# Kernel tuning notes

Hardware: AMD Instinct MI355X
Metric: run time of the kernel (lower is better)

The kernel has to match this reference:

```python
import jax, jax.numpy as jnp
import numpy as np
import math

N_HEADS = 16
KV_HEADS = 4
HEAD_DIM = 128
ROPE_BASE = 1000000.0


def _make_rope(seq_len, dim, base=ROPE_BASE):
    inv_freq = 1.0 / (base ** (np.arange(0, dim, 2, dtype=np.float32) / dim))
    t = np.arange(seq_len, dtype=np.float32)
    freqs = np.outer(t, inv_freq)                     # [S, dim/2]
    emb = np.concatenate([freqs, freqs], axis=-1)     # [S, dim]
    return jnp.asarray(np.cos(emb)), jnp.asarray(np.sin(emb))


def setup_inputs() -> dict:
    key = jax.random.key(0)
    ks = jax.random.split(key, 6)
    B, S, H = 2, 2048, 2048
    kv_dim = KV_HEADS * HEAD_DIM
    s = 1.0 / math.sqrt(H)
    x = jax.random.normal(ks[0], (B, S, H), jnp.float32)
    wq = jax.random.normal(ks[1], (H, H), jnp.float32) * s
    wk = jax.random.normal(ks[2], (kv_dim, H), jnp.float32) * s
    wv = jax.random.normal(ks[3], (kv_dim, H), jnp.float32) * s
    wo = jax.random.normal(ks[4], (H, H), jnp.float32) * s
    bq = jnp.zeros((H,), jnp.float32)
    bk = jnp.zeros((kv_dim,), jnp.float32)
    bv = jnp.zeros((kv_dim,), jnp.float32)
    bo = jnp.zeros((H,), jnp.float32)
    cos, sin = _make_rope(S, HEAD_DIM)
    return {"x": x, "wq": wq, "bq": bq, "wk": wk, "bk": bk,
            "wv": wv, "bv": bv, "wo": wo, "bo": bo, "cos": cos, "sin": sin}


def _rotate_half(t):
    half = t.shape[-1] // 2
    return jnp.concatenate([-t[..., half:], t[..., :half]], axis=-1)


def reference(x, wq, bq, wk, bk, wv, bv, wo, bo, cos, sin):
    B, S, H = x.shape
    hd, nh, kvh = HEAD_DIM, N_HEADS, KV_HEADS
    rep = nh // kvh

    q = (x @ wq.T + bq).reshape(B, S, nh, hd)
    k = (x @ wk.T + bk).reshape(B, S, kvh, hd)
    v = (x @ wv.T + bv).reshape(B, S, kvh, hd)

    # RoPE (rotate-half), cos/sin: [S, hd] -> broadcast over batch and heads
    c = cos[None, :, None, :]
    s_ = sin[None, :, None, :]
    q = q * c + _rotate_half(q) * s_
    k = k * c + _rotate_half(k) * s_

    # GQA: expand KV heads by rep
    k = jnp.repeat(k, rep, axis=2)   # [B, S, nh, hd]
    v = jnp.repeat(v, rep, axis=2)

    q = q.transpose(0, 2, 1, 3)      # [B, nh, S, hd]
    k = k.transpose(0, 2, 1, 3)
    v = v.transpose(0, 2, 1, 3)

    score = jnp.einsum('bhqd,bhkd->bhqk', q, k) / math.sqrt(hd)
    causal = jnp.triu(jnp.full((S, S), -jnp.inf, jnp.float32), k=1)
    score = score + causal
    attn = jax.nn.softmax(score.astype(jnp.float32), axis=-1).astype(q.dtype)

    out = jnp.einsum('bhqk,bhkd->bhqd', attn, v)   # [B, nh, S, hd]
    out = out.transpose(0, 2, 1, 3).reshape(B, S, nh * hd)
    return out @ wo.T + bo
```

## Files before the change

### kernel.cpp

```cpp
#include <hip/hip_runtime.h>

typedef unsigned short u16;
typedef __bf16 bf16x8 __attribute__((ext_vector_type(8)));
typedef float  f32x4  __attribute__((ext_vector_type(4)));

#define SEQ 2048

__device__ __forceinline__ float bf2f(u16 u) {
    union { unsigned int i; float f; } c;
    c.i = ((unsigned int)u) << 16;
    return c.f;
}
__device__ __forceinline__ u16 f2bf(float f) {
    union { float f; unsigned int i; } c;
    c.f = f;
    unsigned int u = c.i;
    u += 0x7FFFu + ((u >> 16) & 1u);
    return (u16)(u >> 16);
}

__device__ __forceinline__ void gl_lds16(const u16* g, u16* l) {
    __builtin_amdgcn_global_load_lds(
        (const __attribute__((address_space(1))) unsigned int*)(g),
        (__attribute__((address_space(3))) unsigned int*)(l), 16, 0, 0);
}

__device__ __forceinline__ void cvt4(const float* s, u16* d) {
    float4 v = *(const float4*)s;
    ushort4 o;
    o.x = f2bf(v.x); o.y = f2bf(v.y); o.z = f2bf(v.z); o.w = f2bf(v.w);
    *(ushort4*)d = o;
}

__global__ void prep(const float* __restrict__ x,
                     const float* __restrict__ wq, const float* __restrict__ wk,
                     const float* __restrict__ wv,
                     const float* __restrict__ bq, const float* __restrict__ bk,
                     const float* __restrict__ bv,
                     u16* __restrict__ xb, u16* __restrict__ wqkvb,
                     float* __restrict__ biasb)
{
    const int E0 = 2097152;
    const int E1 = E0 + 1048576;
    const int E2 = E1 + 262144;
    const int E3 = E2 + 262144;
    const int E4 = E3 + 768;
    int i = blockIdx.x * blockDim.x + threadIdx.x;
    int stride = gridDim.x * blockDim.x;
    for (; i < E4; i += stride) {
        if (i < E0)      cvt4(x  + (size_t)i * 4,        xb    + (size_t)i * 4);
        else if (i < E1) cvt4(wq + (size_t)(i - E0) * 4, wqkvb + (size_t)(i - E0) * 4);
        else if (i < E2) cvt4(wk + (size_t)(i - E1) * 4, wqkvb + 4194304 + (size_t)(i - E1) * 4);
        else if (i < E3) cvt4(wv + (size_t)(i - E2) * 4, wqkvb + 5242880 + (size_t)(i - E2) * 4);
        else {
            int j = i - E3;
            const float* src = (j < 512) ? (bq + j * 4)
                             : (j < 640) ? (bk + (j - 512) * 4)
                                         : (bv + (j - 640) * 4);
            *(float4*)&biasb[j * 4] = *(const float4*)src;
        }
    }
}

__global__ void cvt_f32_bf16(const float* __restrict__ in, u16* __restrict__ out, int n4) {
    int i = blockIdx.x * blockDim.x + threadIdx.x;
    int stride = gridDim.x * blockDim.x;
    for (; i < n4; i += stride) cvt4(in + (size_t)i * 4, out + (size_t)i * 4);
}

template<int MODE>
__global__ __launch_bounds__(256) void gemm_bt(
    const u16* __restrict__ A, const u16* __restrict__ B,
    const float* __restrict__ bias, float* __restrict__ C,
    u16* __restrict__ qb, u16* __restrict__ kb, u16* __restrict__ vt,
    int M, int N, int K)
{
    __shared__ __align__(16) u16 lA[128 * 32];
    __shared__ __align__(16) u16 lB[128 * 32];
    const int tid   = threadIdx.x;
    const int lane  = tid & 63;
    const int wave  = tid >> 6;
    const int waveM = (wave >> 1) * 64;
    const int waveN = (wave & 1) * 64;
    const int bm = blockIdx.x * 128;
    const int bn = blockIdx.y * 128;
    const int lrow = lane & 15;
    const int koff = (lane >> 4) * 8;

    f32x4 acc[4][4] = {};

    for (int k0 = 0; k0 < K; k0 += 32) {
        __syncthreads();
#pragma unroll
        for (int p = 0; p < 2; ++p) {
            int idx = p * 256 + tid;
            int row = idx >> 2;
            int ch  = idx & 3;
            gl_lds16(&A[(size_t)(bm + row) * K + k0 + ch * 8], &lA[(p * 256 + wave * 64) * 8]);
            gl_lds16(&B[(size_t)(bn + row) * K + k0 + ch * 8], &lB[(p * 256 + wave * 64) * 8]);
        }
        __syncthreads();

        bf16x8 af[4], bfr[4];
#pragma unroll
        for (int i = 0; i < 4; ++i)
            af[i] = *(const bf16x8*)&lA[(waveM + i * 16 + lrow) * 32 + koff];
#pragma unroll
        for (int j = 0; j < 4; ++j)
            bfr[j] = *(const bf16x8*)&lB[(waveN + j * 16 + lrow) * 32 + koff];
#pragma unroll
        for (int i = 0; i < 4; ++i)
#pragma unroll
            for (int j = 0; j < 4; ++j)
                acc[i][j] = __builtin_amdgcn_mfma_f32_16x16x32_bf16(
                    af[i], bfr[j], acc[i][j], 0, 0, 0);
    }

    const int r4 = (lane >> 4) * 4;
    const int cn = lane & 15;
#pragma unroll
    for (int i = 0; i < 4; ++i) {
#pragma unroll
        for (int j = 0; j < 4; ++j) {
            int row0 = bm + waveM + i * 16 + r4;
            int col  = bn + waveN + j * 16 + cn;
            float bc = bias[col];
#pragma unroll
            for (int r = 0; r < 4; ++r) {
                float val = acc[i][j][r] + bc;
                if (MODE == 0) {
                    C[(size_t)(row0 + r) * N + col] = val;
                } else {
                    int row = row0 + r;
                    int b = row >> 11;
                    int s = row & 2047;
                    int d = col & 127;
                    u16 o = f2bf(val);
                    if (col < 2048) {
                        int h = col >> 7;
                        qb[(((size_t)(b * 16 + h) * SEQ) + s) * 128 + d] = o;
                    } else if (col < 2560) {
                        int h = (col - 2048) >> 7;
                        kb[(((size_t)(b * 4 + h) * SEQ) + s) * 128 + d] = o;
                    } else {
                        int h = (col - 2560) >> 7;
                        vt[(((size_t)(b * 4 + h) * 128) + d) * SEQ + s] = o;
                    }
                }
            }
        }
    }
}

__global__ void rope_inplace(u16* __restrict__ qb, u16* __restrict__ kb,
                             const float* __restrict__ cosb, const float* __restrict__ sinb)
{
    const int n = (65536 + 16384) * 64;
    int i = blockIdx.x * blockDim.x + threadIdx.x;
    if (i >= n) return;
    int d0  = i & 63;
    int row = i >> 6;
    u16* base;
    if (row < 65536) base = qb + (size_t)row * 128;
    else             base = kb + (size_t)(row - 65536) * 128;
    int s = row & (SEQ - 1);
    float c  = cosb[s * 128 + d0];
    float sn = sinb[s * 128 + d0];
    float a0 = bf2f(base[d0]);
    float a1 = bf2f(base[d0 + 64]);
    base[d0]      = f2bf(a0 * c - a1 * sn);
    base[d0 + 64] = f2bf(a1 * c + a0 * sn);
}

__global__ __launch_bounds__(256, 2) void attn_mfma(
    const u16* __restrict__ qb, const u16* __restrict__ kb,
    const u16* __restrict__ vt, u16* __restrict__ ob)
{
    __shared__ __align__(16) u16 Ks[2][4][64][32];
    __shared__ __align__(16) u16 Vts[2][2][128][32];
    __shared__ __align__(16) u16 Ph[4][16][64];

    const int pair = blockIdx.x;
    const int qA   = pair, qB = 31 - pair;
    const int h    = blockIdx.y;
    const int b    = blockIdx.z;
    const int kvh  = h >> 2;
    const int tid  = threadIdx.x;
    const int lane = tid & 63;
    const int w    = tid >> 6;
    const int c16  = lane & 15;
    const int quad = lane >> 4;
    const float qscale = 0.08838834764831845f * 1.4426950408889634f;

    const u16* kbase  = kb + ((size_t)(b * 4 + kvh) * SEQ) * 128;
    const u16* vtbase = vt + ((size_t)(b * 4 + kvh) * 128) * SEQ;

    bf16x8 qfA[4], qfB[4];
    {
        const u16* qpA = qb + (((size_t)(b * 16 + h)) * SEQ + qA * 64 + w * 16 + c16) * 128;
        const u16* qpB = qb + (((size_t)(b * 16 + h)) * SEQ + qB * 64 + w * 16 + c16) * 128;
#pragma unroll
        for (int kk = 0; kk < 4; ++kk) {
            bf16x8 ta = *(const bf16x8*)(qpA + kk * 32 + quad * 8);
            bf16x8 tb = *(const bf16x8*)(qpB + kk * 32 + quad * 8);
#pragma unroll
            for (int e = 0; e < 8; ++e) {
                ta[e] = (__bf16)((float)ta[e] * qscale);
                tb[e] = (__bf16)((float)tb[e] * qscale);
            }
            qfA[kk] = ta; qfB[kk] = tb;
        }
    }

    int ksrc[4], vsrc[4];
#pragma unroll
    for (int it = 0; it < 4; ++it) {
        int o  = (it * 4 + w) * 1024 + lane * 16;
        int kk = o >> 12;
        int r  = (o >> 6) & 63;
        int c  = (o >> 4) & 3;
        ksrc[it] = r * 128 + kk * 32 + c * 8;
        int p2 = o >> 13;
        int d  = (o >> 6) & 127;
        vsrc[it] = d * SEQ + p2 * 32 + c * 8;
    }

    const int nB = qB + 1;
    const int rowLA = qA * 64 + w * 16 + quad * 4;
    const int rowLB = qB * 64 + w * 16 + quad * 4;

    f32x4 oA[8] = {}, oB[8] = {};
    float lA[4] = {}, lB[4] = {};

    u16* KsF  = &Ks[0][0][0][0];
    u16* VtsF = &Vts[0][0][0][0];

    asm volatile("s_waitcnt vmcnt(0)" ::: "memory");

#pragma unroll
    for (int it = 0; it < 4; ++it) {
        gl_lds16(kbase  + ksrc[it], KsF  + (it * 4 + w) * 512);
        gl_lds16(vtbase + vsrc[it], VtsF + (it * 4 + w) * 512);
    }

    for (int kt = 0; kt < nB; ++kt) {
        const int cur = kt & 1;
        if (kt + 1 < nB) {
            const u16* kg = kbase  + (size_t)(kt + 1) * (64 * 128);
            const u16* vg = vtbase + (kt + 1) * 64;
            u16* kd = KsF  + ((kt + 1) & 1) * (4 * 64 * 32);
            u16* vd = VtsF + ((kt + 1) & 1) * (2 * 128 * 32);
#pragma unroll
            for (int it = 0; it < 4; ++it) {
                gl_lds16(kg + ksrc[it], kd + (it * 4 + w) * 512);
                gl_lds16(vg + vsrc[it], vd + (it * 4 + w) * 512);
            }
            asm volatile("s_waitcnt vmcnt(8)" ::: "memory");
        } else {
            asm volatile("s_waitcnt vmcnt(0)" ::: "memory");
        }
        __builtin_amdgcn_s_barrier();
        asm volatile("" ::: "memory");

        const u16* Kb = KsF  + cur * (4 * 64 * 32);
        const u16* Vb = VtsF + cur * (2 * 128 * 32);
        const bool doA = kt <= qA;

        f32x4 sA[4] = {}, sB[4] = {};
        __builtin_amdgcn_s_setprio(1);
        if (doA) {
#pragma unroll
            for (int kk = 0; kk < 4; ++kk)
#pragma unroll
                for (int j = 0; j < 4; ++j) {
                    bf16x8 kf = *(const bf16x8*)(Kb + (size_t)(kk * 64 + j * 16 + c16) * 32 + quad * 8);
                    sA[j] = __builtin_amdgcn_mfma_f32_16x16x32_bf16(qfA[kk], kf, sA[j], 0, 0, 0);
                    sB[j] = __builtin_amdgcn_mfma_f32_16x16x32_bf16(qfB[kk], kf, sB[j], 0, 0, 0);
                }
        } else {
#pragma unroll
            for (int kk = 0; kk < 4; ++kk)
#pragma unroll
                for (int j = 0; j < 4; ++j) {
                    bf16x8 kf = *(const bf16x8*)(Kb + (size_t)(kk * 64 + j * 16 + c16) * 32 + quad * 8);
                    sB[j] = __builtin_amdgcn_mfma_f32_16x16x32_bf16(qfB[kk], kf, sB[j], 0, 0, 0);
                }
        }
        __builtin_amdgcn_s_setprio(0);

        if (doA && kt == qA) {
#pragma unroll
            for (int j = 0; j < 4; ++j)
#pragma unroll
                for (int rr = 0; rr < 4; ++rr)
                    if (kt * 64 + j * 16 + c16 > rowLA + rr) sA[j][rr] = -1e30f;
        }
        if (kt == qB) {
#pragma unroll
            for (int j = 0; j < 4; ++j)
#pragma unroll
                for (int rr = 0; rr < 4; ++rr)
                    if (kt * 64 + j * 16 + c16 > rowLB + rr) sB[j][rr] = -1e30f;
        }

        bf16x8 paA[2], paB[2];
        if (doA) {
#pragma unroll
            for (int jj = 0; jj < 4; ++jj)
#pragma unroll
                for (int rr = 0; rr < 4; ++rr) {
                    float p = __builtin_amdgcn_exp2f(sA[jj][rr]);
                    lA[rr] += p;
                    int row = quad * 4 + rr;
                    Ph[w][row][(((jj * 2 + (c16 >> 3)) + row) & 7) * 8 + (c16 & 7)] = f2bf(p);
                }
#pragma unroll
            for (int k2 = 0; k2 < 2; ++k2)
                paA[k2] = *(const bf16x8*)&Ph[w][c16][(((k2 * 4 + quad) + c16) & 7) * 8];
        }
#pragma unroll
        for (int jj = 0; jj < 4; ++jj)
#pragma unroll
            for (int rr = 0; rr < 4; ++rr) {
                float p = __builtin_amdgcn_exp2f(sB[jj][rr]);
                lB[rr] += p;
                int row = quad * 4 + rr;
                Ph[w][row][(((jj * 2 + (c16 >> 3)) + row) & 7) * 8 + (c16 & 7)] = f2bf(p);
            }
#pragma unroll
        for (int k2 = 0; k2 < 2; ++k2)
            paB[k2] = *(const bf16x8*)&Ph[w][c16][(((k2 * 4 + quad) + c16) & 7) * 8];

        __builtin_amdgcn_s_setprio(1);
        if (doA) {
#pragma unroll
            for (int k2 = 0; k2 < 2; ++k2)
#pragma unroll
                for (int nt = 0; nt < 8; ++nt) {
                    bf16x8 vf = *(const bf16x8*)(Vb + (size_t)(k2 * 128 + nt * 16 + c16) * 32 + quad * 8);
                    oA[nt] = __builtin_amdgcn_mfma_f32_16x16x32_bf16(paA[k2], vf, oA[nt], 0, 0, 0);
                    oB[nt] = __builtin_amdgcn_mfma_f32_16x16x32_bf16(paB[k2], vf, oB[nt], 0, 0, 0);
                }
        } else {
#pragma unroll
            for (int k2 = 0; k2 < 2; ++k2)
#pragma unroll
                for (int nt = 0; nt < 8; ++nt) {
                    bf16x8 vf = *(const bf16x8*)(Vb + (size_t)(k2 * 128 + nt * 16 + c16) * 32 + quad * 8);
                    oB[nt] = __builtin_amdgcn_mfma_f32_16x16x32_bf16(paB[k2], vf, oB[nt], 0, 0, 0);
                }
        }
        __builtin_amdgcn_s_setprio(0);

        asm volatile("" ::: "memory");
        __builtin_amdgcn_s_barrier();
    }

    float liA[4], liB[4];
#pragma unroll
    for (int rr = 0; rr < 4; ++rr) {
        float la = lA[rr], lb = lB[rr];
        la += __shfl_xor(la, 1); lb += __shfl_xor(lb, 1);
        la += __shfl_xor(la, 2); lb += __shfl_xor(lb, 2);
        la += __shfl_xor(la, 4); lb += __shfl_xor(lb, 4);
        la += __shfl_xor(la, 8); lb += __shfl_xor(lb, 8);
        liA[rr] = 1.0f / la;     liB[rr] = 1.0f / lb;
    }
    const size_t rowGA = (size_t)b * SEQ + rowLA;
    const size_t rowGB = (size_t)b * SEQ + rowLB;
#pragma unroll
    for (int nt = 0; nt < 8; ++nt)
#pragma unroll
        for (int rr = 0; rr < 4; ++rr) {
            ob[(rowGA + rr) * 2048 + h * 128 + nt * 16 + c16] = f2bf(oA[nt][rr] * liA[rr]);
            ob[(rowGB + rr) * 2048 + h * 128 + nt * 16 + c16] = f2bf(oB[nt][rr] * liB[rr]);
        }
}

extern "C" void kernel_launch(void* const* d_in, const int* in_sizes, int n_in,
                              void* d_out, int out_size, void* d_ws, size_t ws_size,
                              hipStream_t stream) {
    const float* x    = (const float*)d_in[0];
    const float* wq   = (const float*)d_in[1];
    const float* bq   = (const float*)d_in[2];
    const float* wk   = (const float*)d_in[3];
    const float* bk   = (const float*)d_in[4];
    const float* wv   = (const float*)d_in[5];
    const float* bv   = (const float*)d_in[6];
    const float* wo   = (const float*)d_in[7];
    const float* bo   = (const float*)d_in[8];
    const float* cosb = (const float*)d_in[9];
    const float* sinb = (const float*)d_in[10];
    float* out = (float*)d_out;

    char* ws = (char*)d_ws;
    const size_t OFF_WQKV = 0;
    const size_t OFF_BIAS = 12582912;
    const size_t OFF_QB   = 12599296;
    const size_t OFF_KB   = 29376512;
    const size_t OFF_VT   = 33570816;
    const size_t OFF_XB   = 37765120;

    u16*   wqkvb = (u16*)(ws + OFF_WQKV);
    u16*   wob   = (u16*)(ws + OFF_WQKV);
    float* biasb = (float*)(ws + OFF_BIAS);
    u16*   qb2   = (u16*)(ws + OFF_QB);
    u16*   kb2   = (u16*)(ws + OFF_KB);
    u16*   vt2   = (u16*)(ws + OFF_VT);
    u16*   xb    = (u16*)(ws + OFF_XB);
    u16*   attnb = (u16*)(ws + OFF_XB);

    prep<<<4096, 256, 0, stream>>>(x, wq, wk, wv, bq, bk, bv, xb, wqkvb, biasb);

    gemm_bt<1><<<dim3(32, 24), 256, 0, stream>>>(xb, wqkvb, biasb, nullptr,
                                                 qb2, kb2, vt2, 4096, 3072, 2048);

    cvt_f32_bf16<<<4096, 256, 0, stream>>>(wo, wob, 1048576);

    rope_inplace<<<((65536 + 16384) * 64) / 256, 256, 0, stream>>>(qb2, kb2, cosb, sinb);

    attn_mfma<<<dim3(16, 16, 2), 256, 0, stream>>>(qb2, kb2, vt2, attnb);

    gemm_bt<0><<<dim3(32, 16), 256, 0, stream>>>(attnb, wob, bo, out,
                                                 nullptr, nullptr, nullptr, 4096, 2048, 2048);
}
```

Measured before the change: 377.9 us.

## Remap attention grid per XCD for K/V L2 reuse and simplify sync

Flattens the attention grid to 1D and decodes the block id so its low three bits select (batch, kv-head). With round-robin dispatch across the 8 XCDs, each XCD then serves the query heads and tiles that share the same K/V, which is meant to raise L2 hit rates. The hand-placed s_waitcnt/s_barrier pipeline and s_setprio hints are replaced by plain __syncthreads, which still lets the next tile's prefetch overlap the current compute. The manual float-to-bf16 rounding for P is replaced by the native __bf16 conversion to cut ALU work. The trade-off is less precise control over wait counts, since a full wait now happens at the end of every iteration.

```diff
diff --git a/kernel.cpp b/kernel.cpp
--- a/kernel.cpp
+++ b/kernel.cpp
@@ -180,11 +180,16 @@
     __shared__ __align__(16) u16 Vts[2][2][128][32];
     __shared__ __align__(16) u16 Ph[4][16][64];
 
-    const int pair = blockIdx.x;
+    const int id   = blockIdx.x;
+    const int s8   = id & 7;
+    const int n    = id >> 3;
+    const int pair = n & 15;
+    const int h_lo = n >> 4;
+    const int b    = s8 >> 2;
+    const int kvh  = s8 & 3;
+    const int h    = kvh * 4 + h_lo;
     const int qA   = pair, qB = 31 - pair;
-    const int h    = blockIdx.y;
-    const int b    = blockIdx.z;
-    const int kvh  = h >> 2;
+
     const int tid  = threadIdx.x;
     const int lane = tid & 63;
     const int w    = tid >> 6;
@@ -235,16 +240,16 @@
     u16* KsF  = &Ks[0][0][0][0];
     u16* VtsF = &Vts[0][0][0][0];
 
-    asm volatile("s_waitcnt vmcnt(0)" ::: "memory");
-
 #pragma unroll
     for (int it = 0; it < 4; ++it) {
         gl_lds16(kbase  + ksrc[it], KsF  + (it * 4 + w) * 512);
         gl_lds16(vtbase + vsrc[it], VtsF + (it * 4 + w) * 512);
     }
+    __syncthreads();
 
     for (int kt = 0; kt < nB; ++kt) {
         const int cur = kt & 1;
+
         if (kt + 1 < nB) {
             const u16* kg = kbase  + (size_t)(kt + 1) * (64 * 128);
             const u16* vg = vtbase + (kt + 1) * 64;
@@ -255,25 +260,17 @@
                 gl_lds16(kg + ksrc[it], kd + (it * 4 + w) * 512);
                 gl_lds16(vg + vsrc[it], vd + (it * 4 + w) * 512);
             }
-            asm volatile("s_waitcnt vmcnt(8)" ::: "memory");
-        } else {
-            asm volatile("s_waitcnt vmcnt(0)" ::: "memory");
-        }
-        __builtin_amdgcn_s_barrier();
-        asm volatile("" ::: "memory");
-
-        const u16* Kb = KsF  + cur * (4 * 64 * 32);
-        const u16* Vb = VtsF + cur * (2 * 128 * 32);
+        }
+
         const bool doA = kt <= qA;
 
         f32x4 sA[4] = {}, sB[4] = {};
-        __builtin_amdgcn_s_setprio(1);
         if (doA) {
 #pragma unroll
             for (int kk = 0; kk < 4; ++kk)
 #pragma unroll
                 for (int j = 0; j < 4; ++j) {
-                    bf16x8 kf = *(const bf16x8*)(Kb + (size_t)(kk * 64 + j * 16 + c16) * 32 + quad * 8);
+                    bf16x8 kf = *(const bf16x8*)&Ks[cur][kk][j * 16 + c16][quad * 8];
                     sA[j] = __builtin_amdgcn_mfma_f32_16x16x32_bf16(qfA[kk], kf, sA[j], 0, 0, 0);
                     sB[j] = __builtin_amdgcn_mfma_f32_16x16x32_bf16(qfB[kk], kf, sB[j], 0, 0, 0);
                 }
@@ -282,11 +279,10 @@
             for (int kk = 0; kk < 4; ++kk)
 #pragma unroll
                 for (int j = 0; j < 4; ++j) {
-                    bf16x8 kf = *(const bf16x8*)(Kb + (size_t)(kk * 64 + j * 16 + c16) * 32 + quad * 8);
+                    bf16x8 kf = *(const bf16x8*)&Ks[cur][kk][j * 16 + c16][quad * 8];
                     sB[j] = __builtin_amdgcn_mfma_f32_16x16x32_bf16(qfB[kk], kf, sB[j], 0, 0, 0);
                 }
         }
-        __builtin_amdgcn_s_setprio(0);
 
         if (doA && kt == qA) {
 #pragma unroll
@@ -312,7 +308,7 @@
                     float p = __builtin_amdgcn_exp2f(sA[jj][rr]);
                     lA[rr] += p;
                     int row = quad * 4 + rr;
-                    Ph[w][row][(((jj * 2 + (c16 >> 3)) + row) & 7) * 8 + (c16 & 7)] = f2bf(p);
+                    *(__bf16*)&Ph[w][row][(((jj * 2 + (c16 >> 3)) + row) & 7) * 8 + (c16 & 7)] = (__bf16)p;
                 }
 #pragma unroll
             for (int k2 = 0; k2 < 2; ++k2)
@@ -325,19 +321,18 @@
                 float p = __builtin_amdgcn_exp2f(sB[jj][rr]);
                 lB[rr] += p;
                 int row = quad * 4 + rr;
-                Ph[w][row][(((jj * 2 + (c16 >> 3)) + row) & 7) * 8 + (c16 & 7)] = f2bf(p);
+                *(__bf16*)&Ph[w][row][(((jj * 2 + (c16 >> 3)) + row) & 7) * 8 + (c16 & 7)] = (__bf16)p;
             }
 #pragma unroll
         for (int k2 = 0; k2 < 2; ++k2)
             paB[k2] = *(const bf16x8*)&Ph[w][c16][(((k2 * 4 + quad) + c16) & 7) * 8];
 
-        __builtin_amdgcn_s_setprio(1);
         if (doA) {
 #pragma unroll
             for (int k2 = 0; k2 < 2; ++k2)
 #pragma unroll
                 for (int nt = 0; nt < 8; ++nt) {
-                    bf16x8 vf = *(const bf16x8*)(Vb + (size_t)(k2 * 128 + nt * 16 + c16) * 32 + quad * 8);
+                    bf16x8 vf = *(const bf16x8*)&Vts[cur][k2][nt * 16 + c16][quad * 8];
                     oA[nt] = __builtin_amdgcn_mfma_f32_16x16x32_bf16(paA[k2], vf, oA[nt], 0, 0, 0);
                     oB[nt] = __builtin_amdgcn_mfma_f32_16x16x32_bf16(paB[k2], vf, oB[nt], 0, 0, 0);
                 }
@@ -346,14 +341,12 @@
             for (int k2 = 0; k2 < 2; ++k2)
 #pragma unroll
                 for (int nt = 0; nt < 8; ++nt) {
-                    bf16x8 vf = *(const bf16x8*)(Vb + (size_t)(k2 * 128 + nt * 16 + c16) * 32 + quad * 8);
+                    bf16x8 vf = *(const bf16x8*)&Vts[cur][k2][nt * 16 + c16][quad * 8];
                     oB[nt] = __builtin_amdgcn_mfma_f32_16x16x32_bf16(paB[k2], vf, oB[nt], 0, 0, 0);
                 }
         }
-        __builtin_amdgcn_s_setprio(0);
-
-        asm volatile("" ::: "memory");
-        __builtin_amdgcn_s_barrier();
+
+        __syncthreads();
     }
 
     float liA[4], liB[4];
@@ -419,7 +412,7 @@
 
     rope_inplace<<<((65536 + 16384) * 64) / 256, 256, 0, stream>>>(qb2, kb2, cosb, sinb);
 
-    attn_mfma<<<dim3(16, 16, 2), 256, 0, stream>>>(qb2, kb2, vt2, attnb);
+    attn_mfma<<<512, 256, 0, stream>>>(qb2, kb2, vt2, attnb);
 
     gemm_bt<0><<<dim3(32, 16), 256, 0, stream>>>(attnb, wob, bo, out,
                                                  nullptr, nullptr, nullptr, 4096, 2048, 2048);
```

Result: faster. 347.3 us (-8.1%).
